# Kernel tuning notes

Hardware: AMD Instinct MI355X
Metric: run time of the kernel (lower is better)

The kernel has to match this reference:

```python
import jax, jax.numpy as jnp
import numpy as np

N = 50000      # num_nodes
E = 1000000    # graph edges
EP = 400000    # pos/neg link-pred edges
H = 128        # hidden_dim
C = 768        # chemical_dim
L = 2          # num GCN layers


def setup_inputs() -> dict:
    key = jax.random.key(0)
    ks = jax.random.split(key, 12)
    edge_index = jax.random.randint(ks[0], (2, E), 0, N)
    chemistry = jax.random.normal(ks[1], (N, C), jnp.float32)
    pos_edge = jax.random.randint(ks[2], (EP, 2), 0, N)
    neg_edge = jax.random.randint(ks[3], (EP, 2), 0, N)
    smiles_mask = jax.random.uniform(ks[4], (N,), jnp.float32)
    node_emb = jax.random.normal(ks[5], (N, H), jnp.float32) * 0.1
    conv_w = jax.random.normal(ks[6], (L, H, H), jnp.float32) / np.sqrt(H)
    conv_b = jnp.zeros((L, H), jnp.float32)
    chem_w = jax.random.normal(ks[7], (C, H), jnp.float32) / np.sqrt(C)
    chem_b = jnp.zeros((H,), jnp.float32)
    dec_w1 = jax.random.normal(ks[8], (2 * H, H), jnp.float32) / np.sqrt(2 * H)
    dec_b1 = jnp.zeros((H,), jnp.float32)
    dec_w2 = jax.random.normal(ks[9], (H, 1), jnp.float32) / np.sqrt(H)
    dec_b2 = jnp.zeros((1,), jnp.float32)
    return dict(edge_index=edge_index, chemistry=chemistry, pos_edge=pos_edge,
                neg_edge=neg_edge, smiles_mask=smiles_mask, node_emb=node_emb,
                conv_w=conv_w, conv_b=conv_b, chem_w=chem_w, chem_b=chem_b,
                dec_w1=dec_w1, dec_b1=dec_b1, dec_w2=dec_w2, dec_b2=dec_b2)


def reference(edge_index, chemistry, pos_edge, neg_edge, smiles_mask, node_emb,
              conv_w, conv_b, chem_w, chem_b, dec_w1, dec_b1, dec_w2, dec_b2):
    row, col = edge_index[0], edge_index[1]  # src -> dst
    # GCN symmetric normalization (add_self_loops=False)
    deg = jax.ops.segment_sum(jnp.ones((E,), jnp.float32), col, num_segments=N)
    dinv = jnp.where(deg > 0, 1.0 / jnp.sqrt(jnp.maximum(deg, 1.0)), 0.0)
    norm = dinv[row] * dinv[col]  # [E]

    # Encoder: structure-only GCN over learned node embeddings
    z = node_emb
    for l in range(L):
        h = z @ conv_w[l]                       # [N,H]
        msg = h[row] * norm[:, None]            # gather [E,H]
        agg = jax.ops.segment_sum(msg, col, num_segments=N)  # scatter-add
        z = jax.nn.relu(agg + conv_b[l])

    # Chemistry projection, masked by smiles validity
    c = jax.nn.relu(chemistry @ chem_w + chem_b) * smiles_mask[:, None]  # [N,H]

    def decode(edges):
        src, dst = edges[:, 0], edges[:, 1]
        f = jnp.concatenate([z[src] * z[dst], c[src] * c[dst]], axis=-1)  # [Ep,2H]
        hmid = jax.nn.relu(f @ dec_w1 + dec_b1)
        return (hmid @ dec_w2 + dec_b2)[:, 0]

    return decode(pos_edge), decode(neg_edge)
```

## Files before the change

### kernel.cpp

```cpp
#include <hip/hip_runtime.h>
#include <hip/hip_fp16.h>

#define NN 50000
#define NE 1000000
#define NEP 400000
#define HD 128
#define CD 768
#define NB_SCAN 196
#define FSTR 256
#define NBKT 196
#define PBLK 2048
#define NPB ((2 * NEP + PBLK - 1) / PBLK)

typedef _Float16 f16x8 __attribute__((ext_vector_type(8)));
typedef _Float16 f16x2 __attribute__((ext_vector_type(2)));
typedef __fp16 hf16x2 __attribute__((ext_vector_type(2)));
typedef __attribute__((ext_vector_type(4))) float f32x4;

__device__ __forceinline__ unsigned pk2h(float a, float b) {
    hf16x2 p = __builtin_amdgcn_cvt_pkrtz(a, b);
    return __builtin_bit_cast(unsigned, p);
}
__device__ __forceinline__ ushort f2h(float x) {
    return (ushort)(pk2h(x, 0.f) & 0xffffu);
}
__device__ __forceinline__ unsigned h2mul(unsigned a, unsigned b) {
    f16x2 ha = __builtin_bit_cast(f16x2, a);
    f16x2 hb = __builtin_bit_cast(f16x2, b);
    f16x2 r = ha * hb;
    return __builtin_bit_cast(unsigned, r);
}
__device__ __forceinline__ f16x8 pack8h(float4 a0, float4 a1) {
    union { unsigned u[4]; f16x8 v; } r;
    r.u[0] = pk2h(a0.x, a0.y);
    r.u[1] = pk2h(a0.z, a0.w);
    r.u[2] = pk2h(a1.x, a1.y);
    r.u[3] = pk2h(a1.z, a1.w);
    return r.v;
}
__device__ __forceinline__ float2 h2f2(unsigned u) {
    f16x2 h = __builtin_bit_cast(f16x2, u);
    return make_float2((float)h[0], (float)h[1]);
}

__global__ __launch_bounds__(256) void count_kernel(const int* __restrict__ col,
                                                    int* __restrict__ cnt) {
    int i = blockIdx.x * 256 + threadIdx.x;
    if (i < NE) atomicAdd(&cnt[col[i]], 1);
}

__global__ __launch_bounds__(256) void scan1_kernel(const int* __restrict__ cnt,
                                                    int* __restrict__ partial,
                                                    int* __restrict__ bsum,
                                                    float* __restrict__ dinv) {
    __shared__ int s[256];
    int i = blockIdx.x * 256 + threadIdx.x;
    int v = (i < NN) ? cnt[i] : 0;
    if (i < NN) dinv[i] = (v > 0) ? 1.0f / sqrtf((float)v) : 0.0f;
    s[threadIdx.x] = v;
    __syncthreads();
    for (int o = 1; o < 256; o <<= 1) {
        int t = (threadIdx.x >= o) ? s[threadIdx.x - o] : 0;
        __syncthreads();
        s[threadIdx.x] += t;
        __syncthreads();
    }
    if (i < NN) partial[i] = s[threadIdx.x] - v;
    if (threadIdx.x == 255) bsum[blockIdx.x] = s[255];
}

__global__ __launch_bounds__(256) void scan2_kernel(int* __restrict__ bsum) {
    __shared__ int s[256];
    int v = (threadIdx.x < NB_SCAN) ? bsum[threadIdx.x] : 0;
    s[threadIdx.x] = v;
    __syncthreads();
    for (int o = 1; o < 256; o <<= 1) {
        int t = (threadIdx.x >= o) ? s[threadIdx.x - o] : 0;
        __syncthreads();
        s[threadIdx.x] += t;
        __syncthreads();
    }
    if (threadIdx.x < NB_SCAN) bsum[threadIdx.x] = s[threadIdx.x] - v;
}

__global__ __launch_bounds__(256) void scan3_kernel(const int* __restrict__ partial,
                                                    const int* __restrict__ bsum,
                                                    int* __restrict__ off,
                                                    int* __restrict__ cursor) {
    int i = blockIdx.x * 256 + threadIdx.x;
    if (i < NN) {
        int o = partial[i] + bsum[blockIdx.x];
        off[i] = o;
        cursor[i] = o;
    }
}

__global__ __launch_bounds__(256) void fill_kernel(const int* __restrict__ row,
                                                   const int* __restrict__ col,
                                                   const float* __restrict__ dinv,
                                                   int* __restrict__ cursor,
                                                   int* __restrict__ csr_idx,
                                                   float* __restrict__ csr_w) {
    int e = blockIdx.x * 256 + threadIdx.x;
    if (e < NE) {
        int c = col[e], r = row[e];
        int slot = atomicAdd(&cursor[c], 1);
        csr_idx[slot] = r;
        csr_w[slot] = dinv[r];
    }
}

__global__ __launch_bounds__(256) void ehist_kernel(const int* __restrict__ pos,
                                                    const int* __restrict__ neg,
                                                    int* __restrict__ bh,
                                                    int* __restrict__ bcnt) {
    __shared__ int h[NBKT];
    const int t = threadIdx.x;
    if (t < NBKT) h[t] = 0;
    __syncthreads();
    const int base = blockIdx.x * PBLK;
#pragma unroll
    for (int j = 0; j < 8; ++j) {
        int i = base + t + j * 256;
        if (i < 2 * NEP) {
            int s = (i < NEP) ? pos[2 * i] : neg[2 * (i - NEP)];
            atomicAdd(&h[s >> 8], 1);
        }
    }
    __syncthreads();
    if (t < NBKT) {
        bh[blockIdx.x * NBKT + t] = h[t];
        if (h[t]) atomicAdd(&bcnt[t], h[t]);
    }
}

__global__ __launch_bounds__(256) void escan_kernel(const int* __restrict__ bcnt,
                                                    int* __restrict__ base) {
    __shared__ int s[256];
    const int t = threadIdx.x;
    int v = (t < NBKT) ? bcnt[t] : 0;
    s[t] = v;
    __syncthreads();
    for (int o = 1; o < 256; o <<= 1) {
        int x = (t >= o) ? s[t - o] : 0;
        __syncthreads();
        s[t] += x;
        __syncthreads();
    }
    if (t < NBKT) base[t] = s[t] - v;
}

__global__ __launch_bounds__(256) void bscan_kernel(const int* __restrict__ bh,
                                                    int* __restrict__ obh) {
    __shared__ int p[256];
    const int b = blockIdx.x;
    const int t = threadIdx.x;
    int v0 = (2 * t < NPB) ? bh[(size_t)(2 * t) * NBKT + b] : 0;
    int v1 = (2 * t + 1 < NPB) ? bh[(size_t)(2 * t + 1) * NBKT + b] : 0;
    p[t] = v0 + v1;
    __syncthreads();
    for (int o = 1; o < 256; o <<= 1) {
        int x = (t >= o) ? p[t - o] : 0;
        __syncthreads();
        p[t] += x;
        __syncthreads();
    }
    int excl = (t > 0) ? p[t - 1] : 0;
    if (2 * t < NPB) obh[(size_t)(2 * t) * NBKT + b] = excl;
    if (2 * t + 1 < NPB) obh[(size_t)(2 * t + 1) * NBKT + b] = excl + v0;
}

__global__ __launch_bounds__(256) void epermute_kernel(const int* __restrict__ pos,
                                                       const int* __restrict__ neg,
                                                       const int* __restrict__ base,
                                                       const int* __restrict__ obh,
                                                       uint2* __restrict__ sd,
                                                       int* __restrict__ oidx) {
    __shared__ int cur[NBKT];
    const int t = threadIdx.x;
    if (t < NBKT) cur[t] = base[t] + obh[(size_t)blockIdx.x * NBKT + t];
    __syncthreads();
    const int bb = blockIdx.x * PBLK;
#pragma unroll
    for (int j = 0; j < 8; ++j) {
        int i = bb + t + j * 256;
        if (i < 2 * NEP) {
            int s, d;
            if (i < NEP) { s = pos[2 * i]; d = pos[2 * i + 1]; }
            else { s = neg[2 * (i - NEP)]; d = neg[2 * (i - NEP) + 1]; }
            int slot = atomicAdd(&cur[s >> 8], 1);
            sd[slot] = make_uint2((unsigned)s, (unsigned)d);
            oidx[slot] = i;
        }
    }
}

__global__ __launch_bounds__(256) void wfrag_all_kernel(const float* __restrict__ w1,
                                                        const float* __restrict__ wc,
                                                        const float* __restrict__ w0,
                                                        const float* __restrict__ wl1,
                                                        ushort* __restrict__ w1f,
                                                        ushort* __restrict__ wcf,
                                                        ushort* __restrict__ wc0f,
                                                        ushort* __restrict__ wc1f) {
    int tid = blockIdx.x * 256 + threadIdx.x;
    int g = tid >> 9;
    const float* w;
    ushort* wf;
    int ks;
    if (g < 8) { w = w1; wf = w1f; ks = g; }
    else if (g < 32) { w = wc; wf = wcf; ks = g - 8; }
    else if (g < 36) { w = w0; wf = wc0f; ks = g - 32; }
    else { w = wl1; wf = wc1f; ks = g - 36; }
    int nt = (tid >> 6) & 7, l = tid & 63;
    int kbase = ks * 32 + ((l >> 4) << 3);
    int colq = nt * 16 + (l & 15);
    ushort r[8];
#pragma unroll
    for (int j = 0; j < 8; ++j) r[j] = f2h(w[(size_t)(kbase + j) * HD + colq]);
    *(uint4*)&wf[(size_t)((ks * 8 + nt) * 64 + l) * 8] = *(uint4*)r;
}

template <int KS, bool EPI>
__global__ __launch_bounds__(256) void feat_mfma_kernel(const float* __restrict__ A,
                                                        const ushort* __restrict__ wf,
                                                        const float* __restrict__ bias,
                                                        const float* __restrict__ mask,
                                                        ushort* __restrict__ out,
                                                        int ostride, int ooff) {
    __shared__ float At[2][64][36];
    const int t = threadIdx.x;
    const int w = t >> 6, lane = t & 63;
    const int rowBase = blockIdx.x * 64;
    const int nt0 = w * 2;
    const int K = KS * 32;

    const int sr0 = t >> 3, sr1 = 32 + (t >> 3), sc4 = (t & 7) * 4;
    const int g0 = rowBase + sr0, g1 = rowBase + sr1;

    float4 p0 = make_float4(0.f, 0.f, 0.f, 0.f), p1 = p0;
    if (g0 < NN) p0 = *(const float4*)&A[(size_t)g0 * K + sc4];
    if (g1 < NN) p1 = *(const float4*)&A[(size_t)g1 * K + sc4];

    f32x4 acc[4][2] = {};

    for (int ks = 0; ks < KS; ++ks) {
        const int b = ks & 1;
        *(float4*)&At[b][sr0][sc4] = p0;
        *(float4*)&At[b][sr1][sc4] = p1;
        __syncthreads();
        if (ks + 1 < KS) {
            p0 = make_float4(0.f, 0.f, 0.f, 0.f); p1 = p0;
            if (g0 < NN) p0 = *(const float4*)&A[(size_t)g0 * K + (ks + 1) * 32 + sc4];
            if (g1 < NN) p1 = *(const float4*)&A[(size_t)g1 * K + (ks + 1) * 32 + sc4];
        }
        f16x8 bf0 = ((const f16x8*)wf)[(ks * 8 + nt0) * 64 + lane];
        f16x8 bf1 = ((const f16x8*)wf)[(ks * 8 + nt0 + 1) * 64 + lane];
#pragma unroll
        for (int mt = 0; mt < 4; ++mt) {
            int row = mt * 16 + (lane & 15);
            float4 a0 = *(const float4*)&At[b][row][(lane >> 4) * 8];
            float4 a1 = *(const float4*)&At[b][row][(lane >> 4) * 8 + 4];
            f16x8 af = pack8h(a0, a1);
            acc[mt][0] = __builtin_amdgcn_mfma_f32_16x16x32_f16(af, bf0, acc[mt][0], 0, 0, 0);
            acc[mt][1] = __builtin_amdgcn_mfma_f32_16x16x32_f16(af, bf1, acc[mt][1], 0, 0, 0);
        }
    }

    const int c0 = lane & 15, rq = lane >> 4;
    float bb0 = EPI ? bias[nt0 * 16 + c0] : 0.f;
    float bb1 = EPI ? bias[nt0 * 16 + 16 + c0] : 0.f;
#pragma unroll
    for (int mt = 0; mt < 4; ++mt) {
#pragma unroll
        for (int reg = 0; reg < 4; ++reg) {
            int grow = rowBase + mt * 16 + rq * 4 + reg;
            if (grow < NN) {
                float v0 = acc[mt][0][reg], v1 = acc[mt][1][reg];
                if (EPI) {
                    float m = mask[grow];
                    v0 = fmaxf(v0 + bb0, 0.f) * m;
                    v1 = fmaxf(v1 + bb1, 0.f) * m;
                }
                out[(size_t)grow * ostride + ooff + nt0 * 16 + c0] = f2h(v0);
                out[(size_t)grow * ostride + ooff + nt0 * 16 + 16 + c0] = f2h(v1);
            }
        }
    }
}

__global__ __launch_bounds__(256) void feat_mfma_f16a_kernel(const ushort* __restrict__ A,
                                                             const ushort* __restrict__ wf,
                                                             ushort* __restrict__ out) {
    __shared__ ushort At[2][64][40];
    const int t = threadIdx.x;
    const int w = t >> 6, lane = t & 63;
    const int rowBase = blockIdx.x * 64;
    const int nt0 = w * 2;

    const int sr = t >> 2, sc = (t & 3) * 8;
    const int g = rowBase + sr;

    uint4 p = make_uint4(0, 0, 0, 0);
    if (g < NN) p = *(const uint4*)&A[(size_t)g * HD + sc];

    f32x4 acc[4][2] = {};

    for (int ks = 0; ks < 4; ++ks) {
        const int b = ks & 1;
        *(uint4*)&At[b][sr][sc] = p;
        __syncthreads();
        if (ks + 1 < 4) {
            p = make_uint4(0, 0, 0, 0);
            if (g < NN) p = *(const uint4*)&A[(size_t)g * HD + (ks + 1) * 32 + sc];
        }
        f16x8 bf0 = ((const f16x8*)wf)[(ks * 8 + nt0) * 64 + lane];
        f16x8 bf1 = ((const f16x8*)wf)[(ks * 8 + nt0 + 1) * 64 + lane];
#pragma unroll
        for (int mt = 0; mt < 4; ++mt) {
            int row = mt * 16 + (lane & 15);
            f16x8 af = *(const f16x8*)&At[b][row][(lane >> 4) * 8];
            acc[mt][0] = __builtin_amdgcn_mfma_f32_16x16x32_f16(af, bf0, acc[mt][0], 0, 0, 0);
            acc[mt][1] = __builtin_amdgcn_mfma_f32_16x16x32_f16(af, bf1, acc[mt][1], 0, 0, 0);
        }
    }

    const int c0 = lane & 15, rq = lane >> 4;
#pragma unroll
    for (int mt = 0; mt < 4; ++mt) {
#pragma unroll
        for (int reg = 0; reg < 4; ++reg) {
            int grow = rowBase + mt * 16 + rq * 4 + reg;
            if (grow < NN) {
                out[(size_t)grow * HD + nt0 * 16 + c0] = f2h(acc[mt][0][reg]);
                out[(size_t)grow * HD + nt0 * 16 + 16 + c0] = f2h(acc[mt][1][reg]);
            }
        }
    }
}

__global__ __launch_bounds__(256) void gather_kernel(const int* __restrict__ off,
                                                     const int* __restrict__ cnt,
                                                     const int* __restrict__ csr_idx,
                                                     const float* __restrict__ csr_w,
                                                     const float* __restrict__ dinv,
                                                     const ushort* __restrict__ h,
                                                     const float* __restrict__ bias,
                                                     ushort* __restrict__ zb,
                                                     int ostride) {
    int v = blockIdx.x * 4 + (threadIdx.x >> 6);
    if (v >= NN) return;
    const int lane = threadIdx.x & 63;
    const int half = lane >> 5, sl = lane & 31;
    const int s = off[v];
    const int e = s + cnt[v];
    float4 acc = make_float4(0.f, 0.f, 0.f, 0.f);
    int b = s;
    for (; b + 7 < e; b += 8) {
        int i0 = b + half, i1 = b + 2 + half, i2 = b + 4 + half, i3 = b + 6 + half;
        int r0 = csr_idx[i0], r1 = csr_idx[i1], r2 = csr_idx[i2], r3 = csr_idx[i3];
        uint2 u0 = *(const uint2*)&h[(size_t)r0 * HD + sl * 4];
        uint2 u1 = *(const uint2*)&h[(size_t)r1 * HD + sl * 4];
        uint2 u2 = *(const uint2*)&h[(size_t)r2 * HD + sl * 4];
        uint2 u3 = *(const uint2*)&h[(size_t)r3 * HD + sl * 4];
        float w0 = csr_w[i0], w1 = csr_w[i1], w2 = csr_w[i2], w3 = csr_w[i3];
        float2 a0 = h2f2(u0.x), c0 = h2f2(u0.y);
        float2 a1 = h2f2(u1.x), c1 = h2f2(u1.y);
        float2 a2 = h2f2(u2.x), c2 = h2f2(u2.y);
        float2 a3 = h2f2(u3.x), c3 = h2f2(u3.y);
        acc.x = fmaf(a0.x, w0, acc.x); acc.y = fmaf(a0.y, w0, acc.y);
        acc.z = fmaf(c0.x, w0, acc.z); acc.w = fmaf(c0.y, w0, acc.w);
        acc.x = fmaf(a1.x, w1, acc.x); acc.y = fmaf(a1.y, w1, acc.y);
        acc.z = fmaf(c1.x, w1, acc.z); acc.w = fmaf(c1.y, w1, acc.w);
        acc.x = fmaf(a2.x, w2, acc.x); acc.y = fmaf(a2.y, w2, acc.y);
        acc.z = fmaf(c2.x, w2, acc.z); acc.w = fmaf(c2.y, w2, acc.w);
        acc.x = fmaf(a3.x, w3, acc.x); acc.y = fmaf(a3.y, w3, acc.y);
        acc.z = fmaf(c3.x, w3, acc.z); acc.w = fmaf(c3.y, w3, acc.w);
    }
    for (; b < e; b += 2) {
        int i = b + half;
        if (i < e) {
            int r = csr_idx[i];
            float w = csr_w[i];
            uint2 u = *(const uint2*)&h[(size_t)r * HD + sl * 4];
            float2 a = h2f2(u.x), c = h2f2(u.y);
            acc.x = fmaf(a.x, w, acc.x); acc.y = fmaf(a.y, w, acc.y);
            acc.z = fmaf(c.x, w, acc.z); acc.w = fmaf(c.y, w, acc.w);
        }
    }
    acc.x += __shfl_xor(acc.x, 32);
    acc.y += __shfl_xor(acc.y, 32);
    acc.z += __shfl_xor(acc.z, 32);
    acc.w += __shfl_xor(acc.w, 32);
    if (half == 0) {
        float dv = dinv[v];
        float4 bb = *(const float4*)&bias[sl * 4];
        float o0 = fmaxf(fmaf(acc.x, dv, bb.x), 0.f);
        float o1 = fmaxf(fmaf(acc.y, dv, bb.y), 0.f);
        float o2 = fmaxf(fmaf(acc.z, dv, bb.z), 0.f);
        float o3 = fmaxf(fmaf(acc.w, dv, bb.w), 0.f);
        uint2 pk;
        pk.x = pk2h(o0, o1);
        pk.y = pk2h(o2, o3);
        *(uint2*)&zb[(size_t)v * ostride + sl * 4] = pk;
    }
}

__global__ __launch_bounds__(256, 4) void decode_mfma_kernel(const uint2* __restrict__ sedges,
                                                             const int* __restrict__ soidx,
                                                             const ushort* __restrict__ feat,
                                                             const ushort* __restrict__ w1f,
                                                             const float* __restrict__ b1,
                                                             const float* __restrict__ w2,
                                                             const float* __restrict__ b2,
                                                             float* __restrict__ out) {
    __shared__ ushort Flds[8 * 4 * 64 * 8];
    const int t = threadIdx.x;
    const int w = t >> 6, lane = t & 63;

    const int nwg = gridDim.x;
    const int orig = blockIdx.x;
    const int q = nwg >> 3, r = nwg & 7;
    const int xcd = orig & 7, k = orig >> 3;
    const int wgid = (xcd < r ? xcd * (q + 1) : r * (q + 1) + (xcd - r) * q) + k;
    const int ebase = wgid * 64;

    const int seg = t & 31, eslot = t >> 5;

    uint2 sdv[8];
#pragma unroll
    for (int j = 0; j < 8; ++j) sdv[j] = sedges[ebase + j * 8 + eslot];
    __builtin_amdgcn_sched_barrier(0);
    uint4 av[8], bv[8];
#pragma unroll
    for (int j = 0; j < 8; ++j) {
        av[j] = *(const uint4*)&feat[(size_t)sdv[j].x * FSTR + seg * 8];
        bv[j] = *(const uint4*)&feat[(size_t)sdv[j].y * FSTR + seg * 8];
    }
#pragma unroll
    for (int j = 0; j < 8; ++j) {
        asm volatile("" : "+v"(av[j].x), "+v"(av[j].y), "+v"(av[j].z), "+v"(av[j].w),
                          "+v"(bv[j].x), "+v"(bv[j].y), "+v"(bv[j].z), "+v"(bv[j].w));
    }
    __builtin_amdgcn_sched_barrier(0);
#pragma unroll
    for (int j = 0; j < 8; ++j) {
        int e = j * 8 + eslot;
        uint4 res;
        res.x = h2mul(av[j].x, bv[j].x);
        res.y = h2mul(av[j].y, bv[j].y);
        res.z = h2mul(av[j].z, bv[j].z);
        res.w = h2mul(av[j].w, bv[j].w);
        int ks = seg >> 2;
        int mt = e >> 4;
        int fl = (e & 15) | ((seg & 3) << 4);
        int swz = (seg & 3) | ((ks & 1) << 2);
        ((uint4*)Flds)[(ks * 4 + mt) * 64 + (fl ^ swz)] = res;
    }
    __syncthreads();

    f32x4 acc[4][2] = {};
    const int nt0 = w * 2;
#pragma unroll
    for (int ks = 0; ks < 8; ++ks) {
        f16x8 bf0 = ((const f16x8*)w1f)[(ks * 8 + nt0) * 64 + lane];
        f16x8 bf1 = ((const f16x8*)w1f)[(ks * 8 + nt0 + 1) * 64 + lane];
        const int rswz = ((lane >> 4) & 3) | ((ks & 1) << 2);
#pragma unroll
        for (int mt = 0; mt < 4; ++mt) {
            f16x8 af = ((const f16x8*)Flds)[(ks * 4 + mt) * 64 + (lane ^ rswz)];
            acc[mt][0] = __builtin_amdgcn_mfma_f32_16x16x32_f16(af, bf0, acc[mt][0], 0, 0, 0);
            acc[mt][1] = __builtin_amdgcn_mfma_f32_16x16x32_f16(af, bf1, acc[mt][1], 0, 0, 0);
        }
    }
    __syncthreads();

    float* partf = (float*)Flds;
    const int c0 = lane & 15, rq = lane >> 4;
    float b1v0 = b1[nt0 * 16 + c0], b1v1 = b1[nt0 * 16 + 16 + c0];
    float w2v0 = w2[nt0 * 16 + c0], w2v1 = w2[nt0 * 16 + 16 + c0];
#pragma unroll
    for (int mt = 0; mt < 4; ++mt) {
#pragma unroll
        for (int reg = 0; reg < 4; ++reg) {
            float h0 = fmaxf(acc[mt][0][reg] + b1v0, 0.f);
            float h1 = fmaxf(acc[mt][1][reg] + b1v1, 0.f);
            float p = fmaf(h0, w2v0, h1 * w2v1);
            p += __shfl_xor(p, 1);
            p += __shfl_xor(p, 2);
            p += __shfl_xor(p, 4);
            p += __shfl_xor(p, 8);
            if (c0 == 0) partf[w * 64 + mt * 16 + rq * 4 + reg] = p;
        }
    }
    __syncthreads();
    if (t < 64) {
        out[soidx[ebase + t]] = partf[t] + partf[64 + t] + partf[128 + t] + partf[192 + t] + b2[0];
    }
}

extern "C" void kernel_launch(void* const* d_in, const int* in_sizes, int n_in,
                              void* d_out, int out_size, void* d_ws, size_t ws_size,
                              hipStream_t stream) {
    const int* edge_index = (const int*)d_in[0];
    const float* chemistry = (const float*)d_in[1];
    const int* pos_edge = (const int*)d_in[2];
    const int* neg_edge = (const int*)d_in[3];
    const float* smiles_mask = (const float*)d_in[4];
    const float* node_emb = (const float*)d_in[5];
    const float* conv_w = (const float*)d_in[6];
    const float* conv_b = (const float*)d_in[7];
    const float* chem_w = (const float*)d_in[8];
    const float* chem_b = (const float*)d_in[9];
    const float* dec_w1 = (const float*)d_in[10];
    const float* dec_b1 = (const float*)d_in[11];
    const float* dec_w2 = (const float*)d_in[12];
    const float* dec_b2 = (const float*)d_in[13];
    float* out = (float*)d_out;

    char* ws = (char*)d_ws;
    int* cnt = (int*)(ws + 0);
    int* bcnt = (int*)(ws + 204800);
    float* dinv = (float*)(ws + 208896);
    int* partial = (int*)(ws + 409600);
    int* off = (int*)(ws + 614400);
    int* cursor = (int*)(ws + 819200);
    int* bsum = (int*)(ws + 1024000);
    int* bbase = (int*)(ws + 1026048);
    int* csr_idx = (int*)(ws + 1048576);
    float* csr_w = (float*)(ws + 5242880);
    ushort* bufZh = (ushort*)(ws + 9437184);
    int* bh = (int*)(ws + 22237184);
    int* obh = (int*)(ws + 22657184);
    ushort* hb = (ushort*)(ws + 35037184);
    ushort* feat = (ushort*)(ws + 47837184);
    ushort* w1f = (ushort*)(ws + 73437184);
    ushort* wcf = (ushort*)(ws + 73502720);
    ushort* wc0f = (ushort*)(ws + 73699328);
    ushort* wc1f = (ushort*)(ws + 73732096);
    uint2* sort_sd = (uint2*)(ws + 35037184);
    int* sort_oidx = (int*)(ws + 41437184);

    const int* e_row = edge_index;
    const int* e_col = edge_index + NE;

    hipMemsetAsync(ws, 0, 205824, stream);
    count_kernel<<<(NE + 255) / 256, 256, 0, stream>>>(e_col, cnt);
    scan1_kernel<<<NB_SCAN, 256, 0, stream>>>(cnt, partial, bsum, dinv);
    scan2_kernel<<<1, 256, 0, stream>>>(bsum);
    scan3_kernel<<<NB_SCAN, 256, 0, stream>>>(partial, bsum, off, cursor);
    fill_kernel<<<(NE + 255) / 256, 256, 0, stream>>>(e_row, e_col, dinv, cursor, csr_idx, csr_w);
    wfrag_all_kernel<<<80, 256, 0, stream>>>(dec_w1, chem_w, conv_w, conv_w + HD * HD,
                                             w1f, wcf, wc0f, wc1f);

    const int mmGrid = (NN + 63) / 64;
    const int gaGrid = (NN + 3) / 4;

    feat_mfma_kernel<4, false><<<mmGrid, 256, 0, stream>>>(node_emb, wc0f, nullptr, nullptr, hb, HD, 0);
    gather_kernel<<<gaGrid, 256, 0, stream>>>(off, cnt, csr_idx, csr_w, dinv, hb, conv_b, bufZh, HD);

    feat_mfma_f16a_kernel<<<mmGrid, 256, 0, stream>>>(bufZh, wc1f, hb);
    gather_kernel<<<gaGrid, 256, 0, stream>>>(off, cnt, csr_idx, csr_w, dinv, hb, conv_b + HD, feat, FSTR);

    ehist_kernel<<<NPB, 256, 0, stream>>>(pos_edge, neg_edge, bh, bcnt);
    escan_kernel<<<1, 256, 0, stream>>>(bcnt, bbase);
    bscan_kernel<<<NBKT, 256, 0, stream>>>(bh, obh);
    epermute_kernel<<<NPB, 256, 0, stream>>>(pos_edge, neg_edge, bbase, obh, sort_sd, sort_oidx);

    feat_mfma_kernel<24, true><<<mmGrid, 256, 0, stream>>>(chemistry, wcf, chem_b, smiles_mask, feat, FSTR, HD);

    decode_mfma_kernel<<<2 * NEP / 64, 256, 0, stream>>>(sort_sd, sort_oidx, feat, w1f,
                                                         dec_b1, dec_w2, dec_b2, out);
}
```

Measured before the change: 414.4 us.

## Gather decoder endpoint features directly into LDS via global_load_lds

The decoder kernel now fetches both endpoint feature rows of each edge straight into shared memory with global_load_lds, using an XOR swizzle, and no longer stages them through VGPRs. The elementwise src*dst product moves into the MFMA operand load, so each wave forms its A fragments from two LDS reads. The aim is to cut register pressure and VGPR traffic in the gather phase and let more loads be in flight. The cost is a 64KB LDS buffer, which lowers the occupancy hint from 4 to 2 blocks per CU, and the product is now recomputed inside the MFMA loop.

```diff
diff --git a/kernel.cpp b/kernel.cpp
--- a/kernel.cpp
+++ b/kernel.cpp
@@ -41,6 +41,11 @@
 __device__ __forceinline__ float2 h2f2(unsigned u) {
     f16x2 h = __builtin_bit_cast(f16x2, u);
     return make_float2((float)h[0], (float)h[1]);
+}
+__device__ __forceinline__ void gload_lds16(const void* g, void* l) {
+    __builtin_amdgcn_global_load_lds(
+        (const __attribute__((address_space(1))) unsigned*)g,
+        (__attribute__((address_space(3))) unsigned*)l, 16, 0, 0);
 }
 
 __global__ __launch_bounds__(256) void count_kernel(const int* __restrict__ col,
@@ -406,7 +411,7 @@
     }
 }
 
-__global__ __launch_bounds__(256, 4) void decode_mfma_kernel(const uint2* __restrict__ sedges,
+__global__ __launch_bounds__(256, 2) void decode_mfma_kernel(const uint2* __restrict__ sedges,
                                                              const int* __restrict__ soidx,
                                                              const ushort* __restrict__ feat,
                                                              const ushort* __restrict__ w1f,
@@ -414,7 +419,7 @@
                                                              const float* __restrict__ w2,
                                                              const float* __restrict__ b2,
                                                              float* __restrict__ out) {
-    __shared__ ushort Flds[8 * 4 * 64 * 8];
+    __shared__ ushort Flds[64 * 512];
     const int t = threadIdx.x;
     const int w = t >> 6, lane = t & 63;
 
@@ -425,52 +430,39 @@
     const int wgid = (xcd < r ? xcd * (q + 1) : r * (q + 1) + (xcd - r) * q) + k;
     const int ebase = wgid * 64;
 
-    const int seg = t & 31, eslot = t >> 5;
-
-    uint2 sdv[8];
-#pragma unroll
-    for (int j = 0; j < 8; ++j) sdv[j] = sedges[ebase + j * 8 + eslot];
-    __builtin_amdgcn_sched_barrier(0);
-    uint4 av[8], bv[8];
-#pragma unroll
-    for (int j = 0; j < 8; ++j) {
-        av[j] = *(const uint4*)&feat[(size_t)sdv[j].x * FSTR + seg * 8];
-        bv[j] = *(const uint4*)&feat[(size_t)sdv[j].y * FSTR + seg * 8];
-    }
-#pragma unroll
-    for (int j = 0; j < 8; ++j) {
-        asm volatile("" : "+v"(av[j].x), "+v"(av[j].y), "+v"(av[j].z), "+v"(av[j].w),
-                          "+v"(bv[j].x), "+v"(bv[j].y), "+v"(bv[j].z), "+v"(bv[j].w));
-    }
-    __builtin_amdgcn_sched_barrier(0);
-#pragma unroll
-    for (int j = 0; j < 8; ++j) {
-        int e = j * 8 + eslot;
-        uint4 res;
-        res.x = h2mul(av[j].x, bv[j].x);
-        res.y = h2mul(av[j].y, bv[j].y);
-        res.z = h2mul(av[j].z, bv[j].z);
-        res.w = h2mul(av[j].w, bv[j].w);
-        int ks = seg >> 2;
-        int mt = e >> 4;
-        int fl = (e & 15) | ((seg & 3) << 4);
-        int swz = (seg & 3) | ((ks & 1) << 2);
-        ((uint4*)Flds)[(ks * 4 + mt) * 64 + (fl ^ swz)] = res;
+    const int sd = lane >> 5;
+    const int hb = (lane & 31) * 16;
+    const char* featB = (const char*)feat;
+#pragma unroll
+    for (int it = 0; it < 16; ++it) {
+        int e = w * 16 + it;
+        uint2 sdv = sedges[ebase + e];
+        unsigned node = sd ? sdv.y : sdv.x;
+        const char* src = featB + (size_t)node * 512 + (hb ^ ((e & 7) << 4));
+        gload_lds16(src, (char*)Flds + e * 1024);
     }
     __syncthreads();
 
     f32x4 acc[4][2] = {};
     const int nt0 = w * 2;
+    const char* FldsB = (const char*)Flds;
 #pragma unroll
     for (int ks = 0; ks < 8; ++ks) {
         f16x8 bf0 = ((const f16x8*)w1f)[(ks * 8 + nt0) * 64 + lane];
         f16x8 bf1 = ((const f16x8*)w1f)[(ks * 8 + nt0 + 1) * 64 + lane];
-        const int rswz = ((lane >> 4) & 3) | ((ks & 1) << 2);
 #pragma unroll
         for (int mt = 0; mt < 4; ++mt) {
-            f16x8 af = ((const f16x8*)Flds)[(ks * 4 + mt) * 64 + (lane ^ rswz)];
-            acc[mt][0] = __builtin_amdgcn_mfma_f32_16x16x32_f16(af, bf0, acc[mt][0], 0, 0, 0);
-            acc[mt][1] = __builtin_amdgcn_mfma_f32_16x16x32_f16(af, bf1, acc[mt][1], 0, 0, 0);
+            int e = mt * 16 + (lane & 15);
+            int koff = (ks * 64 + ((lane >> 4) << 4)) ^ ((e & 7) << 4);
+            uint4 sv = *(const uint4*)(FldsB + e * 1024 + koff);
+            uint4 dv = *(const uint4*)(FldsB + e * 1024 + 512 + koff);
+            union { unsigned u[4]; f16x8 v; } afu;
+            afu.u[0] = h2mul(sv.x, dv.x);
+            afu.u[1] = h2mul(sv.y, dv.y);
+            afu.u[2] = h2mul(sv.z, dv.z);
+            afu.u[3] = h2mul(sv.w, dv.w);
+            acc[mt][0] = __builtin_amdgcn_mfma_f32_16x16x32_f16(afu.v, bf0, acc[mt][0], 0, 0, 0);
+            acc[mt][1] = __builtin_amdgcn_mfma_f32_16x16x32_f16(afu.v, bf1, acc[mt][1], 0, 0, 0);
         }
     }
     __syncthreads();
```

Measured after the change: 477.1 us. +15.1%, slower.

## Fold source-side dinv into matmul epilogue and drop per-edge CSR weights

Applied to the files above, without the earlier changes.

The per-edge weight dinv[row] is now applied once per node in the epilogue of the preceding matmul, instead of being stored per CSR slot and multiplied in the gather. This removes the csr_w array, its writes in the fill kernel, and its reads in both gather passes, so the gather becomes a plain sum of rows. The scaled values are stored in fp16 before summation, which can change rounding slightly. Separately, the asm register barrier in the decode kernel is removed, which may change instruction scheduling.

```diff
diff --git a/kernel.cpp b/kernel.cpp
--- a/kernel.cpp
+++ b/kernel.cpp
@@ -97,16 +97,13 @@
 
 __global__ __launch_bounds__(256) void fill_kernel(const int* __restrict__ row,
                                                    const int* __restrict__ col,
-                                                   const float* __restrict__ dinv,
                                                    int* __restrict__ cursor,
-                                                   int* __restrict__ csr_idx,
-                                                   float* __restrict__ csr_w) {
+                                                   int* __restrict__ csr_idx) {
     int e = blockIdx.x * 256 + threadIdx.x;
     if (e < NE) {
         int c = col[e], r = row[e];
         int slot = atomicAdd(&cursor[c], 1);
         csr_idx[slot] = r;
-        csr_w[slot] = dinv[r];
     }
 }
 
@@ -221,11 +218,12 @@
     *(uint4*)&wf[(size_t)((ks * 8 + nt) * 64 + l) * 8] = *(uint4*)r;
 }
 
-template <int KS, bool EPI>
+template <int KS, bool EPI, bool ROWSCALE>
 __global__ __launch_bounds__(256) void feat_mfma_kernel(const float* __restrict__ A,
                                                         const ushort* __restrict__ wf,
                                                         const float* __restrict__ bias,
                                                         const float* __restrict__ mask,
+                                                        const float* __restrict__ rscale,
                                                         ushort* __restrict__ out,
                                                         int ostride, int ooff) {
     __shared__ float At[2][64][36];
@@ -282,6 +280,11 @@
                     v0 = fmaxf(v0 + bb0, 0.f) * m;
                     v1 = fmaxf(v1 + bb1, 0.f) * m;
                 }
+                if (ROWSCALE) {
+                    float rs = rscale[grow];
+                    v0 *= rs;
+                    v1 *= rs;
+                }
                 out[(size_t)grow * ostride + ooff + nt0 * 16 + c0] = f2h(v0);
                 out[(size_t)grow * ostride + ooff + nt0 * 16 + 16 + c0] = f2h(v1);
             }
@@ -291,6 +294,7 @@
 
 __global__ __launch_bounds__(256) void feat_mfma_f16a_kernel(const ushort* __restrict__ A,
                                                              const ushort* __restrict__ wf,
+                                                             const float* __restrict__ rscale,
                                                              ushort* __restrict__ out) {
     __shared__ ushort At[2][64][40];
     const int t = threadIdx.x;
@@ -332,8 +336,9 @@
         for (int reg = 0; reg < 4; ++reg) {
             int grow = rowBase + mt * 16 + rq * 4 + reg;
             if (grow < NN) {
-                out[(size_t)grow * HD + nt0 * 16 + c0] = f2h(acc[mt][0][reg]);
-                out[(size_t)grow * HD + nt0 * 16 + 16 + c0] = f2h(acc[mt][1][reg]);
+                float rs = rscale[grow];
+                out[(size_t)grow * HD + nt0 * 16 + c0] = f2h(acc[mt][0][reg] * rs);
+                out[(size_t)grow * HD + nt0 * 16 + 16 + c0] = f2h(acc[mt][1][reg] * rs);
             }
         }
     }
@@ -342,7 +347,6 @@
 __global__ __launch_bounds__(256) void gather_kernel(const int* __restrict__ off,
                                                      const int* __restrict__ cnt,
                                                      const int* __restrict__ csr_idx,
-                                                     const float* __restrict__ csr_w,
                                                      const float* __restrict__ dinv,
                                                      const ushort* __restrict__ h,
                                                      const float* __restrict__ bias,
@@ -363,29 +367,23 @@
         uint2 u1 = *(const uint2*)&h[(size_t)r1 * HD + sl * 4];
         uint2 u2 = *(const uint2*)&h[(size_t)r2 * HD + sl * 4];
         uint2 u3 = *(const uint2*)&h[(size_t)r3 * HD + sl * 4];
-        float w0 = csr_w[i0], w1 = csr_w[i1], w2 = csr_w[i2], w3 = csr_w[i3];
         float2 a0 = h2f2(u0.x), c0 = h2f2(u0.y);
         float2 a1 = h2f2(u1.x), c1 = h2f2(u1.y);
         float2 a2 = h2f2(u2.x), c2 = h2f2(u2.y);
         float2 a3 = h2f2(u3.x), c3 = h2f2(u3.y);
-        acc.x = fmaf(a0.x, w0, acc.x); acc.y = fmaf(a0.y, w0, acc.y);
-        acc.z = fmaf(c0.x, w0, acc.z); acc.w = fmaf(c0.y, w0, acc.w);
-        acc.x = fmaf(a1.x, w1, acc.x); acc.y = fmaf(a1.y, w1, acc.y);
-        acc.z = fmaf(c1.x, w1, acc.z); acc.w = fmaf(c1.y, w1, acc.w);
-        acc.x = fmaf(a2.x, w2, acc.x); acc.y = fmaf(a2.y, w2, acc.y);
-        acc.z = fmaf(c2.x, w2, acc.z); acc.w = fmaf(c2.y, w2, acc.w);
-        acc.x = fmaf(a3.x, w3, acc.x); acc.y = fmaf(a3.y, w3, acc.y);
-        acc.z = fmaf(c3.x, w3, acc.z); acc.w = fmaf(c3.y, w3, acc.w);
+        acc.x += a0.x + a1.x + a2.x + a3.x;
+        acc.y += a0.y + a1.y + a2.y + a3.y;
+        acc.z += c0.x + c1.x + c2.x + c3.x;
+        acc.w += c0.y + c1.y + c2.y + c3.y;
     }
     for (; b < e; b += 2) {
         int i = b + half;
         if (i < e) {
             int r = csr_idx[i];
-            float w = csr_w[i];
             uint2 u = *(const uint2*)&h[(size_t)r * HD + sl * 4];
             float2 a = h2f2(u.x), c = h2f2(u.y);
-            acc.x = fmaf(a.x, w, acc.x); acc.y = fmaf(a.y, w, acc.y);
-            acc.z = fmaf(c.x, w, acc.z); acc.w = fmaf(c.y, w, acc.w);
+            acc.x += a.x; acc.y += a.y;
+            acc.z += c.x; acc.w += c.y;
         }
     }
     acc.x += __shfl_xor(acc.x, 32);
@@ -436,11 +434,6 @@
     for (int j = 0; j < 8; ++j) {
         av[j] = *(const uint4*)&feat[(size_t)sdv[j].x * FSTR + seg * 8];
         bv[j] = *(const uint4*)&feat[(size_t)sdv[j].y * FSTR + seg * 8];
-    }
-#pragma unroll
-    for (int j = 0; j < 8; ++j) {
-        asm volatile("" : "+v"(av[j].x), "+v"(av[j].y), "+v"(av[j].z), "+v"(av[j].w),
-                          "+v"(bv[j].x), "+v"(bv[j].y), "+v"(bv[j].z), "+v"(bv[j].w));
     }
     __builtin_amdgcn_sched_barrier(0);
 #pragma unroll
@@ -528,7 +521,6 @@
     int* bsum = (int*)(ws + 1024000);
     int* bbase = (int*)(ws + 1026048);
     int* csr_idx = (int*)(ws + 1048576);
-    float* csr_w = (float*)(ws + 5242880);
     ushort* bufZh = (ushort*)(ws + 9437184);
     int* bh = (int*)(ws + 22237184);
     int* obh = (int*)(ws + 22657184);
@@ -549,25 +541,25 @@
     scan1_kernel<<<NB_SCAN, 256, 0, stream>>>(cnt, partial, bsum, dinv);
     scan2_kernel<<<1, 256, 0, stream>>>(bsum);
     scan3_kernel<<<NB_SCAN, 256, 0, stream>>>(partial, bsum, off, cursor);
-    fill_kernel<<<(NE + 255) / 256, 256, 0, stream>>>(e_row, e_col, dinv, cursor, csr_idx, csr_w);
+    fill_kernel<<<(NE + 255) / 256, 256, 0, stream>>>(e_row, e_col, cursor, csr_idx);
     wfrag_all_kernel<<<80, 256, 0, stream>>>(dec_w1, chem_w, conv_w, conv_w + HD * HD,
                                              w1f, wcf, wc0f, wc1f);
 
     const int mmGrid = (NN + 63) / 64;
     const int gaGrid = (NN + 3) / 4;
 
-    feat_mfma_kernel<4, false><<<mmGrid, 256, 0, stream>>>(node_emb, wc0f, nullptr, nullptr, hb, HD, 0);
-    gather_kernel<<<gaGrid, 256, 0, stream>>>(off, cnt, csr_idx, csr_w, dinv, hb, conv_b, bufZh, HD);
-
-    feat_mfma_f16a_kernel<<<mmGrid, 256, 0, stream>>>(bufZh, wc1f, hb);
-    gather_kernel<<<gaGrid, 256, 0, stream>>>(off, cnt, csr_idx, csr_w, dinv, hb, conv_b + HD, feat, FSTR);
+    feat_mfma_kernel<4, false, true><<<mmGrid, 256, 0, stream>>>(node_emb, wc0f, nullptr, nullptr, dinv, hb, HD, 0);
+    gather_kernel<<<gaGrid, 256, 0, stream>>>(off, cnt, csr_idx, dinv, hb, conv_b, bufZh, HD);
+
+    feat_mfma_f16a_kernel<<<mmGrid, 256, 0, stream>>>(bufZh, wc1f, dinv, hb);
+    gather_kernel<<<gaGrid, 256, 0, stream>>>(off, cnt, csr_idx, dinv, hb, conv_b + HD, feat, FSTR);
 
     ehist_kernel<<<NPB, 256, 0, stream>>>(pos_edge, neg_edge, bh, bcnt);
     escan_kernel<<<1, 256, 0, stream>>>(bcnt, bbase);
     bscan_kernel<<<NBKT, 256, 0, stream>>>(bh, obh);
     epermute_kernel<<<NPB, 256, 0, stream>>>(pos_edge, neg_edge, bbase, obh, sort_sd, sort_oidx);
 
-    feat_mfma_kernel<24, true><<<mmGrid, 256, 0, stream>>>(chemistry, wcf, chem_b, smiles_mask, feat, FSTR, HD);
+    feat_mfma_kernel<24, true, false><<<mmGrid, 256, 0, stream>>>(chemistry, wcf, chem_b, smiles_mask, nullptr, feat, FSTR, HD);
 
     decode_mfma_kernel<<<2 * NEP / 64, 256, 0, stream>>>(sort_sd, sort_oidx, feat, w1f,
                                                          dec_b1, dec_w2, dec_b2, out);
```

Measured after the change: 410.9 us, median of 2. No clear change (-0.8%).
